# Kernel optimization log

Measured on AMD Instinct MI355X. Metric: run time of the kernel, lower is better.

## Reference

```python
import jax, jax.numpy as jnp
import numpy as np

RADIUS = 0.1
NSAMPLE = 64
NEVENT = 2048
B, N, D = 4, 16384, 62
CHANNEL = D + 2  # 64


def index_events(events, idx):
    # events: [B, N, C], idx: [B, ...] -> [B, ..., C]
    return jax.vmap(lambda e, i: e[i])(events, idx)


def square_distance(src, dst):
    # src: [B, S, 2], dst: [B, N, 2] -> [B, S, N]
    return (jnp.sum(src ** 2, -1)[:, :, None]
            + jnp.sum(dst ** 2, -1)[:, None, :]
            - 2.0 * jnp.einsum('bsc,bnc->bsn', src, dst))


def research_circle(radius, nsample, xy, new_xy):
    n = xy.shape[1]
    sqrdists = square_distance(new_xy, xy)            # [B, S, N]
    ar = jnp.arange(n, dtype=jnp.int32)
    group_idx = jnp.where(sqrdists > radius ** 2, n, ar)  # out-of-ball -> N (sorts last)
    group_idx = jnp.sort(group_idx, axis=-1)[:, :, :nsample]
    first = group_idx[:, :, :1]
    return jnp.where(group_idx == n, first, group_idx)     # [B, S, nsample]


def reference(xy, events, fps_idx, affine_alpha, affine_beta):
    b, _, c = xy.shape
    new_xy = index_events(xy, fps_idx)                     # [B, S, 2]
    idx = research_circle(RADIUS, NSAMPLE, xy, new_xy)     # [B, S, K]
    grouped_xy = index_events(xy, idx)                     # [B, S, K, 2]
    grouped_events = index_events(events, idx)             # [B, S, K, D]
    # Normalize (normalize='center')
    g = jnp.concatenate([grouped_events, grouped_xy], axis=-1)  # [B, S, K, D+2]
    mean = jnp.mean(g, axis=2, keepdims=True)              # [B, S, 1, C]
    centered = g - mean
    std = jnp.std(centered.reshape(b, -1), axis=-1, ddof=1)[:, None, None, None]
    g = centered / (std + 1e-05)
    new_events = affine_alpha * g + affine_beta            # [B, S, K, 64]
    return new_xy, new_events


def setup_inputs() -> dict:
    key = jax.random.key(0)
    k1, k2, k3 = jax.random.split(key, 3)
    xy = jax.random.uniform(k1, (B, N, 2), dtype=jnp.float32)
    events = jax.random.normal(k2, (B, N, D), dtype=jnp.float32)
    fps_idx = jax.random.randint(k3, (B, NEVENT), 0, N, dtype=jnp.int32)
    affine_alpha = jnp.ones((1, 1, 1, CHANNEL), dtype=jnp.float32)
    affine_beta = jnp.zeros((1, 1, 1, CHANNEL), dtype=jnp.float32)
    return {"xy": xy, "events": events, "fps_idx": fps_idx,
            "affine_alpha": affine_alpha, "affine_beta": affine_beta}
```

## Files before the change

kernel.cpp:

```cpp
#include <hip/hip_runtime.h>
#include <stdint.h>
#include <math.h>

#define NPTS 16384
#define DEV 62
#define NEVENT 2048
#define NSAMPLE 64
#define CH 64
#define NBATCH 4
#define STOT (NBATCH * NEVENT)
#define M_PER_BATCH (NEVENT * NSAMPLE * CH)

#define OUT1_BASE 16384
#define REG_STRIDE (NSAMPLE * CH)
#define SL_MEAN 64
#define SL_INV 128
#define SL_SS 129

__device__ __forceinline__ int swz_query8192(int blk) {
    int x = blk & 7;
    int j = blk >> 3;
    return (x & 3) * NEVENT + (x >> 2) * (NEVENT / 2) + j;
}
__device__ __forceinline__ int swz_group2048(int blk) {
    int x = blk & 7;
    int j = blk >> 3;
    return (x & 3) * (NEVENT / 4) + (x >> 2) * (NEVENT / 8) + j;
}

__global__ __launch_bounds__(256) void knn_stats_kernel(
    const float2* __restrict__ xy,
    const float* __restrict__ ev,
    const int* __restrict__ fps,
    float* __restrict__ out)
{
    int grp  = swz_group2048(blockIdx.x);
    int w    = threadIdx.x >> 6;
    int lane = threadIdx.x & 63;
    int wave = grp * 4 + w;
    int b    = grp >> 9;

    __shared__ int   sidx[4][NSAMPLE];
    __shared__ float ssum[2][256];
    __shared__ float smean[CH];
    __shared__ float swred[4];

    const float2* xyb = xy + b * NPTS;
    int qi = fps[wave];
    float2 q = xyb[qi];
    if (lane == 0) ((float2*)out)[wave] = q;

    float ssq = __fadd_rn(__fmul_rn(q.x, q.x), __fmul_rn(q.y, q.y));
    const float thr = 0.01f;

    int* regidx = (int*)(out + OUT1_BASE + (size_t)wave * REG_STRIDE);
    int m = 0;
    int first = -1;

    for (int base = 0; base < NPTS; base += 256) {
        float2 p0 = xyb[base       + lane];
        float2 p1 = xyb[base +  64 + lane];
        float2 p2 = xyb[base + 128 + lane];
        float2 p3 = xyb[base + 192 + lane];

        auto proc = [&](float2 p, int idxbase) {
            float ssp = __fadd_rn(__fmul_rn(p.x, p.x), __fmul_rn(p.y, p.y));
            float dot = __builtin_fmaf(q.y, p.y, __fmul_rn(q.x, p.x));
            float d   = __fsub_rn(__fadd_rn(ssq, ssp), __fmul_rn(2.0f, dot));
            bool ok = !(d > thr);
            unsigned long long bal = __ballot(ok);
            if (first < 0 && bal != 0ull)
                first = idxbase + (__ffsll((unsigned long long)bal) - 1);
            if (ok) {
                int pos = m + __popcll(bal & ((1ull << lane) - 1ull));
                if (pos < NSAMPLE) {
                    regidx[pos]  = idxbase + lane;
                    sidx[w][pos] = idxbase + lane;
                }
            }
            m += __popcll(bal);
        };
        proc(p0, base);
        proc(p1, base + 64);
        proc(p2, base + 128);
        proc(p3, base + 192);
        if (m >= NSAMPLE) break;
    }
    if (m < NSAMPLE) {
        for (int p = m + lane; p < NSAMPLE; p += 64) {
            regidx[p]  = first;
            sidx[w][p] = first;
        }
    }

    __syncthreads();

    int tid = threadIdx.x;
    int c2 = tid & 31;
    int kq = tid >> 5;
    const float* evb = ev + (size_t)b * NPTS * DEV;

    for (int qq = 0; qq < 4; ++qq) {
        int s = grp * 4 + qq;
        float* reg = out + OUT1_BASE + (size_t)s * REG_STRIDE;

        float g0[8], g1[8];
        float a0 = 0.f, a1 = 0.f;
#pragma unroll
        for (int j = 0; j < 8; ++j) {
            int row = sidx[qq][8 * j + kq];
            float2 v;
            if (c2 < 31) v = *(const float2*)(evb + (size_t)row * DEV + 2 * c2);
            else         v = xyb[row];
            g0[j] = v.x; g1[j] = v.y;
            a0 += v.x;   a1 += v.y;
        }
        ssum[0][tid] = a0;
        ssum[1][tid] = a1;
        __syncthreads();

        if (tid < CH) {
            int which = tid >> 5, cc = tid & 31;
            float t = 0.f;
#pragma unroll
            for (int p = 0; p < 8; ++p) t += ssum[which][p * 32 + cc];
            smean[2 * cc + which] = t * (1.0f / NSAMPLE);
        }
        __syncthreads();

        if (tid < CH) reg[SL_MEAN + tid] = smean[tid];

        float m0 = smean[2 * c2], m1 = smean[2 * c2 + 1];
        float ss = 0.f;
#pragma unroll
        for (int j = 0; j < 8; ++j) {
            float c0 = g0[j] - m0;
            float c1 = g1[j] - m1;
            ss += c0 * c0 + c1 * c1;
        }

        for (int off = 32; off > 0; off >>= 1) ss += __shfl_down(ss, off, 64);
        if ((tid & 63) == 0) swred[tid >> 6] = ss;
        __syncthreads();
        if (tid == 0) reg[SL_SS] = swred[0] + swred[1] + swred[2] + swred[3];
        __syncthreads();
    }
}

__global__ __launch_bounds__(256) void reduce_std_kernel(float* __restrict__ out)
{
    int b = blockIdx.x;
    int tid = threadIdx.x;
    double acc = 0.0;
    for (int i = tid; i < NEVENT; i += 256)
        acc += (double)out[OUT1_BASE + (size_t)(b * NEVENT + i) * REG_STRIDE + SL_SS];
    __shared__ double sd[256];
    __shared__ float sinv;
    sd[tid] = acc;
    __syncthreads();
    for (int off = 128; off > 0; off >>= 1) {
        if (tid < off) sd[tid] += sd[tid + off];
        __syncthreads();
    }
    if (tid == 0) {
        double stdv = sqrt(sd[0] / (double)(M_PER_BATCH - 1));
        sinv = (float)(1.0 / (stdv + 1e-5));
    }
    __syncthreads();
    float inv = sinv;
    for (int i = tid; i < NEVENT; i += 256)
        out[OUT1_BASE + (size_t)(b * NEVENT + i) * REG_STRIDE + SL_INV] = inv;
}

__global__ __launch_bounds__(256) void finalize_kernel(
    const float2* __restrict__ xy,
    const float* __restrict__ ev,
    const float* __restrict__ alpha,
    const float* __restrict__ beta,
    float* __restrict__ out)
{
    int s = swz_query8192(blockIdx.x);
    int b = s >> 11;
    int tid = threadIdx.x;
    float* reg = out + OUT1_BASE + (size_t)s * REG_STRIDE;

    __shared__ int sidx[NSAMPLE];
    __shared__ float sm[CH], sa[CH], sbet[CH];
    __shared__ float sinv;

    if (tid < NSAMPLE) {
        sidx[tid] = ((const int*)reg)[tid];
        sm[tid] = reg[SL_MEAN + tid];
    } else if (tid < 128) {
        sa[tid - 64] = alpha[tid - 64];
        sbet[tid - 64] = beta[tid - 64];
    } else if (tid == 128) {
        sinv = reg[SL_INV];
    }
    __syncthreads();

    int c2 = tid & 31;
    int kq = tid >> 5;
    float inv = sinv;

    const float* evb = ev + (size_t)b * NPTS * DEV;
    const float2* xyb = xy + b * NPTS;

    float m0 = sm[2 * c2],   m1 = sm[2 * c2 + 1];
    float al0 = sa[2 * c2],  al1 = sa[2 * c2 + 1];
    float be0 = sbet[2 * c2], be1 = sbet[2 * c2 + 1];

    float2* outp = (float2*)reg;
#pragma unroll
    for (int j = 0; j < 8; ++j) {
        int row = sidx[8 * j + kq];
        float2 v;
        if (c2 < 31) v = *(const float2*)(evb + (size_t)row * DEV + 2 * c2);
        else         v = xyb[row];
        float2 r;
        r.x = al0 * ((v.x - m0) * inv) + be0;
        r.y = al1 * ((v.y - m1) * inv) + be1;
        outp[256 * j + tid] = r;
    }
}

extern "C" void kernel_launch(void* const* d_in, const int* in_sizes, int n_in,
                              void* d_out, int out_size, void* d_ws, size_t ws_size,
                              hipStream_t stream) {
    const float2* xy    = (const float2*)d_in[0];
    const float*  ev    = (const float*)d_in[1];
    const int*    fps   = (const int*)d_in[2];
    const float*  alpha = (const float*)d_in[3];
    const float*  beta  = (const float*)d_in[4];
    float* out = (float*)d_out;
    (void)d_ws; (void)ws_size;

    knn_stats_kernel<<<STOT / 4, 256, 0, stream>>>(xy, ev, fps, out);
    reduce_std_kernel<<<NBATCH, 256, 0, stream>>>(out);
    finalize_kernel<<<STOT, 256, 0, stream>>>(xy, ev, alpha, beta, out);
}
```

Baseline: 193.8 us.

## Write gathered rows in stats pass and normalize in place in finalize

The stats kernel now writes the gathered event/xy values straight into the output region while computing means, and stores per-query means, sums of squares and the per-batch inverse std in the workspace instead of scratch slots inside the output. The finalize kernel no longer re-gathers from the events tensor by index. It streams the output in place with float4 loads and stores and applies the affine normalization. This replaces a second random gather with a coalesced read-modify-write, at the cost of an extra full write-then-read of the output buffer and a dependency on workspace size.

```diff
diff --git a/kernel.cpp b/kernel.cpp
--- a/kernel.cpp
+++ b/kernel.cpp
@@ -13,15 +13,10 @@
 
 #define OUT1_BASE 16384
 #define REG_STRIDE (NSAMPLE * CH)
-#define SL_MEAN 64
-#define SL_INV 128
-#define SL_SS 129
-
-__device__ __forceinline__ int swz_query8192(int blk) {
-    int x = blk & 7;
-    int j = blk >> 3;
-    return (x & 3) * NEVENT + (x >> 2) * (NEVENT / 2) + j;
-}
+#define WS_MEAN 0
+#define WS_SS   (STOT * CH)
+#define WS_INV  (WS_SS + STOT)
+
 __device__ __forceinline__ int swz_group2048(int blk) {
     int x = blk & 7;
     int j = blk >> 3;
@@ -32,6 +27,7 @@
     const float2* __restrict__ xy,
     const float* __restrict__ ev,
     const int* __restrict__ fps,
+    float* __restrict__ ws,
     float* __restrict__ out)
 {
     int grp  = swz_group2048(blockIdx.x);
@@ -53,7 +49,6 @@
     float ssq = __fadd_rn(__fmul_rn(q.x, q.x), __fmul_rn(q.y, q.y));
     const float thr = 0.01f;
 
-    int* regidx = (int*)(out + OUT1_BASE + (size_t)wave * REG_STRIDE);
     int m = 0;
     int first = -1;
 
@@ -73,10 +68,7 @@
                 first = idxbase + (__ffsll((unsigned long long)bal) - 1);
             if (ok) {
                 int pos = m + __popcll(bal & ((1ull << lane) - 1ull));
-                if (pos < NSAMPLE) {
-                    regidx[pos]  = idxbase + lane;
-                    sidx[w][pos] = idxbase + lane;
-                }
+                if (pos < NSAMPLE) sidx[w][pos] = idxbase + lane;
             }
             m += __popcll(bal);
         };
@@ -87,10 +79,8 @@
         if (m >= NSAMPLE) break;
     }
     if (m < NSAMPLE) {
-        for (int p = m + lane; p < NSAMPLE; p += 64) {
-            regidx[p]  = first;
+        for (int p = m + lane; p < NSAMPLE; p += 64)
             sidx[w][p] = first;
-        }
     }
 
     __syncthreads();
@@ -102,7 +92,7 @@
 
     for (int qq = 0; qq < 4; ++qq) {
         int s = grp * 4 + qq;
-        float* reg = out + OUT1_BASE + (size_t)s * REG_STRIDE;
+        float2* outp = (float2*)(out + OUT1_BASE + (size_t)s * REG_STRIDE);
 
         float g0[8], g1[8];
         float a0 = 0.f, a1 = 0.f;
@@ -114,6 +104,7 @@
             else         v = xyb[row];
             g0[j] = v.x; g1[j] = v.y;
             a0 += v.x;   a1 += v.y;
+            outp[256 * j + tid] = v;
         }
         ssum[0][tid] = a0;
         ssum[1][tid] = a1;
@@ -128,7 +119,7 @@
         }
         __syncthreads();
 
-        if (tid < CH) reg[SL_MEAN + tid] = smean[tid];
+        if (tid < CH) ws[WS_MEAN + (size_t)s * CH + tid] = smean[tid];
 
         float m0 = smean[2 * c2], m1 = smean[2 * c2 + 1];
         float ss = 0.f;
@@ -142,20 +133,19 @@
         for (int off = 32; off > 0; off >>= 1) ss += __shfl_down(ss, off, 64);
         if ((tid & 63) == 0) swred[tid >> 6] = ss;
         __syncthreads();
-        if (tid == 0) reg[SL_SS] = swred[0] + swred[1] + swred[2] + swred[3];
-        __syncthreads();
-    }
-}
-
-__global__ __launch_bounds__(256) void reduce_std_kernel(float* __restrict__ out)
+        if (tid == 0) ws[WS_SS + s] = swred[0] + swred[1] + swred[2] + swred[3];
+        __syncthreads();
+    }
+}
+
+__global__ __launch_bounds__(256) void reduce_std_kernel(float* __restrict__ ws)
 {
     int b = blockIdx.x;
     int tid = threadIdx.x;
     double acc = 0.0;
     for (int i = tid; i < NEVENT; i += 256)
-        acc += (double)out[OUT1_BASE + (size_t)(b * NEVENT + i) * REG_STRIDE + SL_SS];
+        acc += (double)ws[WS_SS + b * NEVENT + i];
     __shared__ double sd[256];
-    __shared__ float sinv;
     sd[tid] = acc;
     __syncthreads();
     for (int off = 128; off > 0; off >>= 1) {
@@ -164,63 +154,46 @@
     }
     if (tid == 0) {
         double stdv = sqrt(sd[0] / (double)(M_PER_BATCH - 1));
-        sinv = (float)(1.0 / (stdv + 1e-5));
-    }
-    __syncthreads();
-    float inv = sinv;
-    for (int i = tid; i < NEVENT; i += 256)
-        out[OUT1_BASE + (size_t)(b * NEVENT + i) * REG_STRIDE + SL_INV] = inv;
+        ws[WS_INV + b] = (float)(1.0 / (stdv + 1e-5));
+    }
 }
 
 __global__ __launch_bounds__(256) void finalize_kernel(
-    const float2* __restrict__ xy,
-    const float* __restrict__ ev,
     const float* __restrict__ alpha,
     const float* __restrict__ beta,
+    const float* __restrict__ ws,
     float* __restrict__ out)
 {
-    int s = swz_query8192(blockIdx.x);
+    int s = blockIdx.x;
     int b = s >> 11;
     int tid = threadIdx.x;
     float* reg = out + OUT1_BASE + (size_t)s * REG_STRIDE;
 
-    __shared__ int sidx[NSAMPLE];
     __shared__ float sm[CH], sa[CH], sbet[CH];
     __shared__ float sinv;
 
-    if (tid < NSAMPLE) {
-        sidx[tid] = ((const int*)reg)[tid];
-        sm[tid] = reg[SL_MEAN + tid];
-    } else if (tid < 128) {
-        sa[tid - 64] = alpha[tid - 64];
-        sbet[tid - 64] = beta[tid - 64];
-    } else if (tid == 128) {
-        sinv = reg[SL_INV];
+    if (tid < CH) {
+        sm[tid]   = ws[WS_MEAN + (size_t)s * CH + tid];
+        sa[tid]   = alpha[tid];
+        sbet[tid] = beta[tid];
+    } else if (tid == CH) {
+        sinv = ws[WS_INV + b];
     }
     __syncthreads();
 
-    int c2 = tid & 31;
-    int kq = tid >> 5;
     float inv = sinv;
-
-    const float* evb = ev + (size_t)b * NPTS * DEV;
-    const float2* xyb = xy + b * NPTS;
-
-    float m0 = sm[2 * c2],   m1 = sm[2 * c2 + 1];
-    float al0 = sa[2 * c2],  al1 = sa[2 * c2 + 1];
-    float be0 = sbet[2 * c2], be1 = sbet[2 * c2 + 1];
-
-    float2* outp = (float2*)reg;
-#pragma unroll
-    for (int j = 0; j < 8; ++j) {
-        int row = sidx[8 * j + kq];
-        float2 v;
-        if (c2 < 31) v = *(const float2*)(evb + (size_t)row * DEV + 2 * c2);
-        else         v = xyb[row];
-        float2 r;
-        r.x = al0 * ((v.x - m0) * inv) + be0;
-        r.y = al1 * ((v.y - m1) * inv) + be1;
-        outp[256 * j + tid] = r;
+    float4* p = (float4*)reg;
+#pragma unroll
+    for (int it = 0; it < 4; ++it) {
+        int e = 256 * it + tid;
+        int c = (4 * e) & 63;
+        float4 v = p[e];
+        float4 r;
+        r.x = sa[c + 0] * ((v.x - sm[c + 0]) * inv) + sbet[c + 0];
+        r.y = sa[c + 1] * ((v.y - sm[c + 1]) * inv) + sbet[c + 1];
+        r.z = sa[c + 2] * ((v.z - sm[c + 2]) * inv) + sbet[c + 2];
+        r.w = sa[c + 3] * ((v.w - sm[c + 3]) * inv) + sbet[c + 3];
+        p[e] = r;
     }
 }
 
@@ -233,9 +206,9 @@
     const float*  alpha = (const float*)d_in[3];
     const float*  beta  = (const float*)d_in[4];
     float* out = (float*)d_out;
-    (void)d_ws; (void)ws_size;
-
-    knn_stats_kernel<<<STOT / 4, 256, 0, stream>>>(xy, ev, fps, out);
-    reduce_std_kernel<<<NBATCH, 256, 0, stream>>>(out);
-    finalize_kernel<<<STOT, 256, 0, stream>>>(xy, ev, alpha, beta, out);
-}
+    float* ws  = (float*)d_ws;
+
+    knn_stats_kernel<<<STOT / 4, 256, 0, stream>>>(xy, ev, fps, ws, out);
+    reduce_std_kernel<<<NBATCH, 256, 0, stream>>>(ws);
+    finalize_kernel<<<STOT, 256, 0, stream>>>(alpha, beta, ws, out);
+}
```

Measured after the change: 217.6 us. 12.2% more time.

## Fold std reduction into finalize kernel, move stats to workspace, nontemporal stores

Applied to the files above, without the earlier changes.

Per-query means and sum-of-squares now go into a separate workspace buffer instead of being stashed inside the output region. The standalone 4-block reduce_std kernel is removed, and each finalize block redundantly recomputes its batch's std reduction from 2048 workspace values. This drops one kernel launch and its serialization, at the cost of 8192 blocks each doing a small double-precision reduction. Output writes also use nontemporal stores to avoid cache pollution.

```diff
diff --git a/kernel.cpp b/kernel.cpp
--- a/kernel.cpp
+++ b/kernel.cpp
@@ -13,9 +13,8 @@
 
 #define OUT1_BASE 16384
 #define REG_STRIDE (NSAMPLE * CH)
-#define SL_MEAN 64
-#define SL_INV 128
-#define SL_SS 129
+#define WS_MEAN 0
+#define WS_SS   (STOT * CH)
 
 __device__ __forceinline__ int swz_query8192(int blk) {
     int x = blk & 7;
@@ -32,6 +31,7 @@
     const float2* __restrict__ xy,
     const float* __restrict__ ev,
     const int* __restrict__ fps,
+    float* __restrict__ ws,
     float* __restrict__ out)
 {
     int grp  = swz_group2048(blockIdx.x);
@@ -102,7 +102,6 @@
 
     for (int qq = 0; qq < 4; ++qq) {
         int s = grp * 4 + qq;
-        float* reg = out + OUT1_BASE + (size_t)s * REG_STRIDE;
 
         float g0[8], g1[8];
         float a0 = 0.f, a1 = 0.f;
@@ -128,7 +127,7 @@
         }
         __syncthreads();
 
-        if (tid < CH) reg[SL_MEAN + tid] = smean[tid];
+        if (tid < CH) ws[WS_MEAN + (size_t)s * CH + tid] = smean[tid];
 
         float m0 = smean[2 * c2], m1 = smean[2 * c2 + 1];
         float ss = 0.f;
@@ -142,34 +141,9 @@
         for (int off = 32; off > 0; off >>= 1) ss += __shfl_down(ss, off, 64);
         if ((tid & 63) == 0) swred[tid >> 6] = ss;
         __syncthreads();
-        if (tid == 0) reg[SL_SS] = swred[0] + swred[1] + swred[2] + swred[3];
-        __syncthreads();
-    }
-}
-
-__global__ __launch_bounds__(256) void reduce_std_kernel(float* __restrict__ out)
-{
-    int b = blockIdx.x;
-    int tid = threadIdx.x;
-    double acc = 0.0;
-    for (int i = tid; i < NEVENT; i += 256)
-        acc += (double)out[OUT1_BASE + (size_t)(b * NEVENT + i) * REG_STRIDE + SL_SS];
-    __shared__ double sd[256];
-    __shared__ float sinv;
-    sd[tid] = acc;
-    __syncthreads();
-    for (int off = 128; off > 0; off >>= 1) {
-        if (tid < off) sd[tid] += sd[tid + off];
-        __syncthreads();
-    }
-    if (tid == 0) {
-        double stdv = sqrt(sd[0] / (double)(M_PER_BATCH - 1));
-        sinv = (float)(1.0 / (stdv + 1e-5));
-    }
-    __syncthreads();
-    float inv = sinv;
-    for (int i = tid; i < NEVENT; i += 256)
-        out[OUT1_BASE + (size_t)(b * NEVENT + i) * REG_STRIDE + SL_INV] = inv;
+        if (tid == 0) ws[WS_SS + s] = swred[0] + swred[1] + swred[2] + swred[3];
+        __syncthreads();
+    }
 }
 
 __global__ __launch_bounds__(256) void finalize_kernel(
@@ -177,6 +151,7 @@
     const float* __restrict__ ev,
     const float* __restrict__ alpha,
     const float* __restrict__ beta,
+    const float* __restrict__ ws,
     float* __restrict__ out)
 {
     int s = swz_query8192(blockIdx.x);
@@ -186,16 +161,29 @@
 
     __shared__ int sidx[NSAMPLE];
     __shared__ float sm[CH], sa[CH], sbet[CH];
+    __shared__ double sd[256];
     __shared__ float sinv;
 
     if (tid < NSAMPLE) {
         sidx[tid] = ((const int*)reg)[tid];
-        sm[tid] = reg[SL_MEAN + tid];
+        sm[tid]   = ws[WS_MEAN + (size_t)s * CH + tid];
     } else if (tid < 128) {
-        sa[tid - 64] = alpha[tid - 64];
+        sa[tid - 64]   = alpha[tid - 64];
         sbet[tid - 64] = beta[tid - 64];
-    } else if (tid == 128) {
-        sinv = reg[SL_INV];
+    }
+
+    double acc = 0.0;
+    for (int i = tid; i < NEVENT; i += 256)
+        acc += (double)ws[WS_SS + b * NEVENT + i];
+    sd[tid] = acc;
+    __syncthreads();
+    for (int off = 128; off > 0; off >>= 1) {
+        if (tid < off) sd[tid] += sd[tid + off];
+        __syncthreads();
+    }
+    if (tid == 0) {
+        double stdv = sqrt(sd[0] / (double)(M_PER_BATCH - 1));
+        sinv = (float)(1.0 / (stdv + 1e-5));
     }
     __syncthreads();
 
@@ -220,7 +208,9 @@
         float2 r;
         r.x = al0 * ((v.x - m0) * inv) + be0;
         r.y = al1 * ((v.y - m1) * inv) + be1;
-        outp[256 * j + tid] = r;
+        float* pp = (float*)&outp[256 * j + tid];
+        __builtin_nontemporal_store(r.x, pp);
+        __builtin_nontemporal_store(r.y, pp + 1);
     }
 }
 
@@ -233,9 +223,8 @@
     const float*  alpha = (const float*)d_in[3];
     const float*  beta  = (const float*)d_in[4];
     float* out = (float*)d_out;
-    (void)d_ws; (void)ws_size;
-
-    knn_stats_kernel<<<STOT / 4, 256, 0, stream>>>(xy, ev, fps, out);
-    reduce_std_kernel<<<NBATCH, 256, 0, stream>>>(out);
-    finalize_kernel<<<STOT, 256, 0, stream>>>(xy, ev, alpha, beta, out);
-}
+    float* ws  = (float*)d_ws;
+
+    knn_stats_kernel<<<STOT / 4, 256, 0, stream>>>(xy, ev, fps, ws, out);
+    finalize_kernel<<<STOT, 256, 0, stream>>>(xy, ev, alpha, beta, ws, out);
+}
```

Result: no change. 196.3 us (+1.3%).
